# Optimization experiments

Measured on AMD Instinct MI355X. Metric: run time of the kernel, lower is better.

The kernel has to match this reference:

```python
import jax, jax.numpy as jnp
import numpy as np

BS, SL, FD = 8192, 49, 11
D_MODEL, DM2, HEAD = 128, 64, 8
NH, NHID, NLAYER = DM2 // HEAD, 4, 2
ABF = 1.0
XY_IDX = np.array([0, 1, 2, 3, 4, 5, 6, 7, 10])  # x feats + y feat (batch-normed cols)
DEC_IN = D_MODEL + 10  # d_model + len(x_dims + spa_dims)


def tanhshrink(x):
    return x - jnp.tanh(x)


def rope_angles(spa):
    # spa: [bs, sl, 2] -> per-token block angles [bs, sl, 4]
    # block order matches torch.block_diag(Rx(t0), Ry(t0), Rx(t1), Ry(t1))
    thetas = 10000.0 ** ((2.0 - 2.0 * jnp.arange(2, dtype=spa.dtype)) / 8.0)  # d=8, n_thetas=2
    ax = spa[..., 0:1] * thetas  # [bs, sl, 2]
    ay = spa[..., 1:2] * thetas
    return jnp.stack([ax[..., 0], ay[..., 0], ax[..., 1], ay[..., 1]], axis=-1)


def apply_rope(v, ang):
    # v: [bs, nh, s, 8]; ang: [bs, s, 4]. Applies the 8x8 block-diagonal
    # rotation directly on 2-d sub-pairs (same math as R @ v, no 8x8 matmats).
    c = jnp.cos(ang)[:, None]  # [bs, 1, s, 4]
    s = jnp.sin(ang)[:, None]
    v2 = v.reshape(*v.shape[:-1], 4, 2)
    r = jnp.stack([c * v2[..., 0] - s * v2[..., 1],
                   s * v2[..., 0] + c * v2[..., 1]], axis=-1)
    return r.reshape(v.shape)


def heads(x):  # [bs, s, dm2] -> [bs, nh, s, hd]
    b, s, _ = x.shape
    return x.reshape(b, s, NH, HEAD).transpose(0, 2, 1, 3)


def merge(x):  # [bs, nh, s, hd] -> [bs, s, dm2]
    b, h, s, d = x.shape
    return x.transpose(0, 2, 1, 3).reshape(b, s, h * d)


def mlp2(x, w1, b1, w2, b2):
    return tanhshrink(x @ w1 + b1) @ w2 + b2


def forward_impl(input_tensor, dists, bn_gamma, bn_beta,
                 xe_w1, xe_b1, xe_w2, xe_b2, ye_w1, ye_b1, ye_w2, ye_b2,
                 learnable_y, hidden_tokens, Wq, Wk, Wv, Wo, Wq2, Wk2, Wv2, Wo2,
                 dec_w0, dec_b0, dec_w1, dec_b1, dec_w2, dec_b2):
    bs = input_tensor.shape[0]
    # --- NanBatchNorm over x+y feature columns (no NaNs in clean inputs) ---
    xy = input_tensor[:, :, XY_IDX]
    mu = jnp.mean(xy, axis=(0, 1), keepdims=True)
    var = jnp.var(xy, axis=(0, 1), keepdims=True)
    xy = (xy - mu) / jnp.sqrt(var + 1e-5) * bn_gamma + bn_beta
    input_tensor = input_tensor.at[:, :, XY_IDX].set(xy)

    # --- target at last seq position: drop its dist, keep context dists ---
    dists_ctx = dists[:, :-1]                       # [bs, sl-1]
    central_x = input_tensor[:, -1:, :-1]           # [bs, 1, 10] (x + spa feats)

    # --- 2D RoPE angles from spatial coords ---
    ang = rope_angles(input_tensor[:, :, 8:10])     # [bs, sl, 4]

    # --- FCN encoders (two streams a=x, b=y) ---
    x_embed = mlp2(input_tensor[:, :, :8], xe_w1, xe_b1, xe_w2, xe_b2)      # [bs, sl, 64]
    y_embed = mlp2(input_tensor[:, :-1, 10:11], ye_w1, ye_b1, ye_w2, ye_b2)  # [bs, sl-1, 64]
    y_embed = jnp.concatenate([y_embed, jnp.broadcast_to(learnable_y, (bs, 1, DM2))], axis=1)

    ctx = (x_embed[:, :-1], y_embed[:, :-1])
    qry = (x_embed[:, -1:], y_embed[:, -1:])
    ang_ctx, ang_q = ang[:, :-1], ang[:, -1:]
    bias = (-ABF * dists_ctx)[:, None, None, :]     # [bs, 1, 1, sl-1]
    scale = 1.0 / jnp.sqrt(jnp.asarray(HEAD, input_tensor.dtype))

    outs, attn_ws = [], []
    for s in range(2):
        H = jnp.broadcast_to(hidden_tokens, (bs, NHID, DM2))
        for l in range(NLAYER):
            q = heads(H @ Wq[l, s])
            k = apply_rope(heads(ctx[s] @ Wk[l, s]), ang_ctx)
            v = heads(ctx[s] @ Wv[l, s])
            sc = jnp.einsum('bhqd,bhkd->bhqk', q, k) * scale + bias
            a = jax.nn.softmax(sc, axis=-1)
            H = H + merge(jnp.einsum('bhqk,bhkd->bhqd', a, v)) @ Wo[l, s]
        # query cross-attends the inducing tokens
        q = apply_rope(heads(qry[s] @ Wq2[s]), ang_q)
        k = heads(H @ Wk2[s])
        v = heads(H @ Wv2[s])
        sc = jnp.einsum('bhqd,bhkd->bhqk', q, k) * scale
        a = jax.nn.softmax(sc, axis=-1)
        outs.append(merge(jnp.einsum('bhqk,bhkd->bhqd', a, v)) @ Wo2[s])  # [bs, 1, 64]
        attn_ws.append(a)

    encoding = jnp.concatenate(outs, axis=-1)               # [bs, 1, 128]
    encoding = jnp.concatenate([encoding, central_x], axis=-1)  # [bs, 1, 138]
    h = tanhshrink(encoding @ dec_w0 + dec_b0)
    h = tanhshrink(h @ dec_w1 + dec_b1)
    pred = h @ dec_w2 + dec_b2                              # [bs, 1, 1]
    return pred


def setup_inputs() -> dict:
    key = jax.random.key(0)
    ks = jax.random.split(key, 32)
    g = lambda i, shape: 0.05 * jax.random.normal(ks[i], shape, dtype=jnp.float32)
    inp = {
        'input_tensor': jax.random.normal(ks[0], (BS, SL, FD), dtype=jnp.float32),
        'dists': jax.random.uniform(ks[1], (BS, SL), dtype=jnp.float32),
        'target_position': jnp.zeros((3, BS), dtype=jnp.int32),
        'bn_gamma': jnp.ones((9,), jnp.float32),
        'bn_beta': jnp.zeros((9,), jnp.float32),
        'xe_w1': g(2, (8, DM2)), 'xe_b1': jnp.zeros((DM2,), jnp.float32),
        'xe_w2': g(3, (DM2, DM2)), 'xe_b2': jnp.zeros((DM2,), jnp.float32),
        'ye_w1': g(4, (1, DM2)), 'ye_b1': jnp.zeros((DM2,), jnp.float32),
        'ye_w2': g(5, (DM2, DM2)), 'ye_b2': jnp.zeros((DM2,), jnp.float32),
        'learnable_y': g(6, (1, 1, DM2)),
        'hidden_tokens': g(7, (NHID, DM2)),
        'Wq': g(8, (NLAYER, 2, DM2, DM2)), 'Wk': g(9, (NLAYER, 2, DM2, DM2)),
        'Wv': g(10, (NLAYER, 2, DM2, DM2)), 'Wo': g(11, (NLAYER, 2, DM2, DM2)),
        'Wq2': g(12, (2, DM2, DM2)), 'Wk2': g(13, (2, DM2, DM2)),
        'Wv2': g(14, (2, DM2, DM2)), 'Wo2': g(15, (2, DM2, DM2)),
        'dec_w0': g(16, (DEC_IN, 512)), 'dec_b0': jnp.zeros((512,), jnp.float32),
        'dec_w1': g(17, (512, 256)), 'dec_b1': jnp.zeros((256,), jnp.float32),
        'dec_w2': g(18, (256, 1)), 'dec_b2': jnp.zeros((1,), jnp.float32),
    }
    return inp


def reference(input_tensor, dists, target_position, bn_gamma, bn_beta,
              xe_w1, xe_b1, xe_w2, xe_b2, ye_w1, ye_b1, ye_w2, ye_b2,
              learnable_y, hidden_tokens, Wq, Wk, Wv, Wo, Wq2, Wk2, Wv2, Wo2,
              dec_w0, dec_b0, dec_w1, dec_b1, dec_w2, dec_b2):
    # target_position is an index constant (query is the last token by construction)
    return forward_impl(input_tensor, dists, bn_gamma, bn_beta,
                        xe_w1, xe_b1, xe_w2, xe_b2, ye_w1, ye_b1, ye_w2, ye_b2,
                        learnable_y, hidden_tokens, Wq, Wk, Wv, Wo, Wq2, Wk2, Wv2, Wo2,
                        dec_w0, dec_b0, dec_w1, dec_b1, dec_w2, dec_b2)
```

## Files before the change

kernel.cpp:

```cpp
#include <hip/hip_runtime.h>
#include <math.h>

#define BS 8192
#define SL 49
#define FDIM 11
#define ROWS (BS*SL)

__device__ __forceinline__ float tanhshrink_f(float x) {
  float e = __expf(2.f * x);
  return (x - 1.f) + __fdividef(2.f, e + 1.f);
}

__global__ __launch_bounds__(256) void k_stats(const float* __restrict__ inp,
                                               double* __restrict__ gsum) {
  const int nblk = gridDim.x;
  const int per = (ROWS + nblk - 1) / nblk;
  const int r0 = blockIdx.x * per;
  int r1 = r0 + per; if (r1 > ROWS) r1 = ROWS;
  float s[9], q[9];
#pragma unroll
  for (int j = 0; j < 9; ++j) { s[j] = 0.f; q[j] = 0.f; }
  for (int r = r0 + threadIdx.x; r < r1; r += 256) {
    const float* row = inp + r * FDIM;
#pragma unroll
    for (int j = 0; j < 9; ++j) {
      float v = row[j < 8 ? j : 10];
      s[j] += v; q[j] += v * v;
    }
  }
#pragma unroll
  for (int j = 0; j < 9; ++j) {
    for (int off = 32; off; off >>= 1) {
      s[j] += __shfl_down(s[j], off);
      q[j] += __shfl_down(q[j], off);
    }
  }
  __shared__ float red[4][18];
  const int wid = threadIdx.x >> 6;
  const int lane = threadIdx.x & 63;
  if (lane == 0) {
#pragma unroll
    for (int j = 0; j < 9; ++j) { red[wid][j] = s[j]; red[wid][9 + j] = q[j]; }
  }
  __syncthreads();
  if (threadIdx.x < 18) {
    float t = red[0][threadIdx.x] + red[1][threadIdx.x] +
              red[2][threadIdx.x] + red[3][threadIdx.x];
    atomicAdd(&gsum[threadIdx.x], (double)t);
  }
}

__global__ __launch_bounds__(256) void k_finalize(const double* __restrict__ gsum,
                           const float* __restrict__ gamma,
                           const float* __restrict__ beta,
                           const float* __restrict__ hidden,
                           const float* __restrict__ Wq,
                           float* __restrict__ bnp,
                           float* __restrict__ q0g) {
  int tid = threadIdx.x;
  if (tid < 9) {
    const double N = (double)ROWS;
    double mean = gsum[tid] / N;
    double msq  = gsum[9 + tid] / N;
    float var = (float)(msq - mean * mean);
    float sc = gamma[tid] / sqrtf(var + 1e-5f);
    bnp[tid] = sc;
    bnp[9 + tid] = beta[tid] - (float)mean * sc;
  }
  int s = tid >> 7, i2 = (tid >> 6) & 1, c = tid & 63;
  const float* W = Wq + (s << 12);
#pragma unroll
  for (int ii = 0; ii < 2; ++ii) {
    int i = i2 + 2 * ii;
    float a = 0.f;
    for (int k = 0; k < 64; ++k) a += hidden[i * 64 + k] * W[k * 64 + c];
    q0g[s * 256 + i * 64 + c] = a;
  }
}

__global__ __launch_bounds__(256, 4) void k_mega(
    const float* __restrict__ inp, const float* __restrict__ dists,
    const float* __restrict__ bnp, const float* __restrict__ q0g,
    const float* __restrict__ xe_w1, const float* __restrict__ xe_b1,
    const float* __restrict__ xe_w2, const float* __restrict__ xe_b2,
    const float* __restrict__ ye_w1, const float* __restrict__ ye_b1,
    const float* __restrict__ ye_w2, const float* __restrict__ ye_b2,
    const float* __restrict__ learnable_y, const float* __restrict__ hidden_tokens,
    const float* __restrict__ Wq, const float* __restrict__ Wk,
    const float* __restrict__ Wv, const float* __restrict__ Wo,
    const float* __restrict__ Wq2, const float* __restrict__ Wk2,
    const float* __restrict__ Wv2, const float* __restrict__ Wo2,
    float* __restrict__ enc)
{
  __shared__ float raw[49][12];
  __shared__ float cs8[49][8];
  __shared__ float emb[49][64];
  __shared__ float KB[49][68];
  __shared__ float scb[32][52];
  __shared__ float Hs[4][64];
  __shared__ float qb[4][64];
  __shared__ float db[48];
  __shared__ float bnl[18];
  __shared__ float q2[64];
  __shared__ float o1[64];
  __shared__ float a2[32];

  const int tid  = threadIdx.x;
  const int lane = tid & 63;
  const int grp  = tid >> 6;
  const int b    = blockIdx.x >> 1;
  const int s    = blockIdx.x & 1;
  const float scale = 0.35355339059327373f;

  for (int i = tid; i < 49 * FDIM; i += 256) raw[i / FDIM][i % FDIM] = inp[b * (49*FDIM) + i];
  if (tid < 18) bnl[tid] = bnp[tid];
  if (tid >= 64 && tid < 112) db[tid - 64] = dists[b * 49 + (tid - 64)];
  __syncthreads();

  if (tid < 49) {
    float x = raw[tid][8], y = raw[tid][9];
    cs8[tid][0] = cosf(10.f * x); cs8[tid][1] = cosf(10.f * y);
    cs8[tid][2] = cosf(x);        cs8[tid][3] = cosf(y);
    cs8[tid][4] = sinf(10.f * x); cs8[tid][5] = sinf(10.f * y);
    cs8[tid][6] = sinf(x);        cs8[tid][7] = sinf(y);
  }
  for (int i = tid; i < 441; i += 256) {
    int t = i / 9, j = i - t * 9;
    int f = (j < 8) ? j : 10;
    raw[t][f] = raw[t][f] * bnl[j] + bnl[9 + j];
  }
  __syncthreads();

  if (s == 0 && tid < 10) enc[b * 138 + 128 + tid] = raw[48][tid];

  if (s == 0) {
    const float bias1 = xe_b1[lane];
    float acc[13];
#pragma unroll
    for (int j = 0; j < 13; ++j) acc[j] = bias1;
#pragma unroll
    for (int k = 0; k < 8; ++k) {
      float w = xe_w1[k * 64 + lane];
#pragma unroll
      for (int j = 0; j < 13; ++j) {
        int t = grp + 4 * j;
        if (t < 49) acc[j] += raw[t][k] * w;
      }
    }
#pragma unroll
    for (int j = 0; j < 13; ++j) {
      int t = grp + 4 * j;
      if (t < 49) KB[t][lane] = tanhshrink_f(acc[j]);
    }
  } else {
    const float w1y = ye_w1[lane];
    const float b1y = ye_b1[lane];
#pragma unroll
    for (int j = 0; j < 12; ++j) {
      int t = grp + 4 * j;
      KB[t][lane] = tanhshrink_f(raw[t][10] * w1y + b1y);
    }
  }

  if (s == 0) {
    const float b2 = xe_b2[lane];
    float acc[13];
#pragma unroll
    for (int j = 0; j < 13; ++j) acc[j] = b2;
    for (int k = 0; k < 64; k += 4) {
      float w0 = xe_w2[(k + 0) * 64 + lane];
      float w1_ = xe_w2[(k + 1) * 64 + lane];
      float w2_ = xe_w2[(k + 2) * 64 + lane];
      float w3_ = xe_w2[(k + 3) * 64 + lane];
#pragma unroll
      for (int j = 0; j < 13; ++j) {
        int t = grp + 4 * j;
        if (t < 49) {
          float4 cv = *(const float4*)&KB[t][k];
          acc[j] += cv.x * w0 + cv.y * w1_ + cv.z * w2_ + cv.w * w3_;
        }
      }
    }
#pragma unroll
    for (int j = 0; j < 13; ++j) {
      int t = grp + 4 * j;
      if (t < 49) emb[t][lane] = acc[j];
    }
  } else {
    const float b2 = ye_b2[lane];
    float acc[12];
#pragma unroll
    for (int j = 0; j < 12; ++j) acc[j] = b2;
    for (int k = 0; k < 64; k += 4) {
      float w0 = ye_w2[(k + 0) * 64 + lane];
      float w1_ = ye_w2[(k + 1) * 64 + lane];
      float w2_ = ye_w2[(k + 2) * 64 + lane];
      float w3_ = ye_w2[(k + 3) * 64 + lane];
#pragma unroll
      for (int j = 0; j < 12; ++j) {
        float4 cv = *(const float4*)&KB[grp + 4 * j][k];
        acc[j] += cv.x * w0 + cv.y * w1_ + cv.z * w2_ + cv.w * w3_;
      }
    }
#pragma unroll
    for (int j = 0; j < 12; ++j) emb[grp + 4 * j][lane] = acc[j];
    if (tid < 64) emb[48][lane] = learnable_y[lane];
  }
  Hs[grp][lane] = hidden_tokens[grp * 64 + lane];

#pragma unroll 1
  for (int l = 0; l < 2; ++l) {
    const float* Wk_p = Wk + ((l * 2 + s) << 12);
    const float* Wv_p = Wv + ((l * 2 + s) << 12);
    const float* Wo_p = Wo + ((l * 2 + s) << 12);
    if (l == 0) {
      qb[grp][lane] = q0g[s * 256 + tid];
    } else {
      const float* Wq_p = Wq + ((l * 2 + s) << 12);
      float a = 0.f;
      for (int k = 0; k < 64; k += 4) {
        float4 hv = *(const float4*)&Hs[grp][k];
        a += hv.x * Wq_p[(k + 0) * 64 + lane] + hv.y * Wq_p[(k + 1) * 64 + lane]
           + hv.z * Wq_p[(k + 2) * 64 + lane] + hv.w * Wq_p[(k + 3) * 64 + lane];
      }
      qb[grp][lane] = a;
    }
    {
      float aK[12];
#pragma unroll
      for (int j = 0; j < 12; ++j) aK[j] = 0.f;
      for (int k = 0; k < 64; k += 4) {
        float wk0 = Wk_p[(k + 0) * 64 + lane], wk1 = Wk_p[(k + 1) * 64 + lane];
        float wk2 = Wk_p[(k + 2) * 64 + lane], wk3 = Wk_p[(k + 3) * 64 + lane];
#pragma unroll
        for (int j = 0; j < 12; ++j) {
          float4 cv = *(const float4*)&emb[grp + 4 * j][k];
          aK[j] += cv.x * wk0 + cv.y * wk1 + cv.z * wk2 + cv.w * wk3;
        }
      }
      const int p = (lane >> 1) & 3;
      const int odd = lane & 1;
#pragma unroll
      for (int j = 0; j < 12; ++j) {
        int t = grp + 4 * j;
        float other = __shfl_xor(aK[j], 1);
        float co = cs8[t][p], si = cs8[t][4 + p];
        KB[t][lane] = odd ? (si * other + co * aK[j]) : (co * aK[j] - si * other);
      }
    }
    __syncthreads();
    {
      const int t0 = tid & 7;
      const int i  = (tid >> 3) & 3;
      const int h  = tid >> 5;
      const int r  = tid >> 3;
      float4 qa = *(const float4*)&qb[i][h * 8];
      float4 qc = *(const float4*)&qb[i][h * 8 + 4];
      float v[6];
#pragma unroll
      for (int j = 0; j < 6; ++j) {
        int t = t0 + 8 * j;
        float4 ka = *(const float4*)&KB[t][h * 8];
        float4 kc = *(const float4*)&KB[t][h * 8 + 4];
        float a = qa.x * ka.x + qa.y * ka.y + qa.z * ka.z + qa.w * ka.w
                + qc.x * kc.x + qc.y * kc.y + qc.z * kc.z + qc.w * kc.w;
        v[j] = a * scale - db[t];
      }
      float m = fmaxf(fmaxf(fmaxf(v[0], v[1]), fmaxf(v[2], v[3])), fmaxf(v[4], v[5]));
      m = fmaxf(m, __shfl_xor(m, 1));
      m = fmaxf(m, __shfl_xor(m, 2));
      m = fmaxf(m, __shfl_xor(m, 4));
      float sum = 0.f;
#pragma unroll
      for (int j = 0; j < 6; ++j) { v[j] = __expf(v[j] - m); sum += v[j]; }
      sum += __shfl_xor(sum, 1);
      sum += __shfl_xor(sum, 2);
      sum += __shfl_xor(sum, 4);
      float inv = 1.f / sum;
#pragma unroll
      for (int j = 0; j < 6; ++j) scb[r][t0 + 8 * j] = v[j] * inv;
    }
    __syncthreads();
    {
      float acc[8];
#pragma unroll
      for (int m = 0; m < 8; ++m) acc[m] = 0.f;
      for (int tt = 0; tt < 48; tt += 4) {
        float e0 = emb[tt + 0][lane], e1 = emb[tt + 1][lane];
        float e2 = emb[tt + 2][lane], e3 = emb[tt + 3][lane];
#pragma unroll
        for (int m = 0; m < 8; ++m) {
          float4 sc4 = *(const float4*)&scb[grp + 4 * m][tt];
          acc[m] += sc4.x * e0 + sc4.y * e1 + sc4.z * e2 + sc4.w * e3;
        }
      }
#pragma unroll
      for (int m = 0; m < 8; ++m) KB[grp + 4 * m][lane] = acc[m];
    }
    {
      const int r = ((lane >> 3) << 2) + grp;
      float a = 0.f;
      for (int c = 0; c < 64; c += 4) {
        float4 tv = *(const float4*)&KB[r][c];
        a += tv.x * Wv_p[(c + 0) * 64 + lane] + tv.y * Wv_p[(c + 1) * 64 + lane]
           + tv.z * Wv_p[(c + 2) * 64 + lane] + tv.w * Wv_p[(c + 3) * 64 + lane];
      }
      qb[grp][lane] = a;
    }
    {
      float a = Hs[grp][lane];
      for (int k = 0; k < 64; k += 4) {
        float4 av = *(const float4*)&qb[grp][k];
        a += av.x * Wo_p[(k + 0) * 64 + lane] + av.y * Wo_p[(k + 1) * 64 + lane]
           + av.z * Wo_p[(k + 2) * 64 + lane] + av.w * Wo_p[(k + 3) * 64 + lane];
      }
      Hs[grp][lane] = a;
    }
  }

  const float* Wq2_p = Wq2 + (s << 12);
  const float* Wk2_p = Wk2 + (s << 12);
  const float* Wv2_p = Wv2 + (s << 12);
  const float* Wo2_p = Wo2 + (s << 12);
  if (tid < 64) {
    float a = 0.f;
    for (int k = 0; k < 64; k += 4) {
      float4 cv = *(const float4*)&emb[48][k];
      a += cv.x * Wq2_p[(k + 0) * 64 + lane] + cv.y * Wq2_p[(k + 1) * 64 + lane]
         + cv.z * Wq2_p[(k + 2) * 64 + lane] + cv.w * Wq2_p[(k + 3) * 64 + lane];
    }
    float other = __shfl_xor(a, 1);
    int p = (lane >> 1) & 3;
    float co = cs8[48][p], si = cs8[48][4 + p];
    q2[lane] = (lane & 1) ? (si * other + co * a) : (co * a - si * other);
  }
  {
    float aK = 0.f, aV = 0.f;
    for (int k = 0; k < 64; k += 4) {
      float4 hv = *(const float4*)&Hs[grp][k];
      aK += hv.x * Wk2_p[(k + 0) * 64 + lane] + hv.y * Wk2_p[(k + 1) * 64 + lane]
          + hv.z * Wk2_p[(k + 2) * 64 + lane] + hv.w * Wk2_p[(k + 3) * 64 + lane];
      aV += hv.x * Wv2_p[(k + 0) * 64 + lane] + hv.y * Wv2_p[(k + 1) * 64 + lane]
          + hv.z * Wv2_p[(k + 2) * 64 + lane] + hv.w * Wv2_p[(k + 3) * 64 + lane];
    }
    KB[grp][lane] = aK;
    KB[8 + grp][lane] = aV;
  }
  __syncthreads();
  if (tid < 32) {
    int h = tid >> 2, i = tid & 3;
    float a = 0.f;
#pragma unroll
    for (int d = 0; d < 8; ++d) a += q2[h * 8 + d] * KB[i][h * 8 + d];
    a *= scale;
    float m = fmaxf(a, __shfl_xor(a, 1));
    m = fmaxf(m, __shfl_xor(m, 2));
    float e = __expf(a - m);
    float sum = e + __shfl_xor(e, 1);
    sum += __shfl_xor(sum, 2);
    a2[tid] = e / sum;
  }
  if (tid < 64) {
    int h = lane >> 3;
    float a = 0.f;
#pragma unroll
    for (int i = 0; i < 4; ++i) a += a2[h * 4 + i] * KB[8 + i][lane];
    o1[lane] = a;
  }
  if (tid < 64) {
    float a = 0.f;
    for (int k = 0; k < 64; k += 4) {
      float4 ov = *(const float4*)&o1[k];
      a += ov.x * Wo2_p[(k + 0) * 64 + lane] + ov.y * Wo2_p[(k + 1) * 64 + lane]
         + ov.z * Wo2_p[(k + 2) * 64 + lane] + ov.w * Wo2_p[(k + 3) * 64 + lane];
    }
    enc[b * 138 + s * 64 + lane] = a;
  }
}

__global__ __launch_bounds__(256, 5) void k_dec(
    const float* __restrict__ enc,
    const float* __restrict__ w0, const float* __restrict__ b0,
    const float* __restrict__ w1, const float* __restrict__ b1,
    const float* __restrict__ w2, const float* __restrict__ b2,
    float* __restrict__ out)
{
  __shared__ float encs[8][140];
  __shared__ float h0s[8][512];
  __shared__ float h1s[8][256];
  const int tid = threadIdx.x;
  const int rb = blockIdx.x * 8;

  for (int i = tid; i < 8 * 138; i += 256) {
    int r = i / 138, k = i - r * 138;
    encs[r][k] = enc[(rb + r) * 138 + k];
  }
  __syncthreads();
  {
    float acc0[8], acc1[8];
    const float bb0 = b0[tid], bb1 = b0[tid + 256];
#pragma unroll
    for (int r = 0; r < 8; ++r) { acc0[r] = bb0; acc1[r] = bb1; }
    for (int k = 0; k < 136; k += 4) {
      float wa0 = w0[(k + 0) * 512 + tid], wa1 = w0[(k + 1) * 512 + tid];
      float wa2 = w0[(k + 2) * 512 + tid], wa3 = w0[(k + 3) * 512 + tid];
      float wb0 = w0[(k + 0) * 512 + tid + 256], wb1 = w0[(k + 1) * 512 + tid + 256];
      float wb2 = w0[(k + 2) * 512 + tid + 256], wb3 = w0[(k + 3) * 512 + tid + 256];
#pragma unroll
      for (int r = 0; r < 8; ++r) {
        float4 ev = *(const float4*)&encs[r][k];
        acc0[r] += ev.x * wa0 + ev.y * wa1 + ev.z * wa2 + ev.w * wa3;
        acc1[r] += ev.x * wb0 + ev.y * wb1 + ev.z * wb2 + ev.w * wb3;
      }
    }
    for (int k = 136; k < 138; ++k) {
      float wa = w0[k * 512 + tid], wb = w0[k * 512 + tid + 256];
#pragma unroll
      for (int r = 0; r < 8; ++r) {
        float e = encs[r][k];
        acc0[r] += e * wa; acc1[r] += e * wb;
      }
    }
#pragma unroll
    for (int r = 0; r < 8; ++r) {
      h0s[r][tid] = tanhshrink_f(acc0[r]);
      h0s[r][tid + 256] = tanhshrink_f(acc1[r]);
    }
  }
  __syncthreads();
  {
    float acc[8];
    const float bb = b1[tid];
#pragma unroll
    for (int r = 0; r < 8; ++r) acc[r] = bb;
    for (int k = 0; k < 512; k += 4) {
      float ww0 = w1[(k + 0) * 256 + tid], ww1 = w1[(k + 1) * 256 + tid];
      float ww2 = w1[(k + 2) * 256 + tid], ww3 = w1[(k + 3) * 256 + tid];
#pragma unroll
      for (int r = 0; r < 8; ++r) {
        float4 hv = *(const float4*)&h0s[r][k];
        acc[r] += hv.x * ww0 + hv.y * ww1 + hv.z * ww2 + hv.w * ww3;
      }
    }
#pragma unroll
    for (int r = 0; r < 8; ++r) h1s[r][tid] = tanhshrink_f(acc[r]);
  }
  __syncthreads();
  {
    int r = tid >> 5, l32 = tid & 31;
    float a = 0.f;
#pragma unroll
    for (int kk = 0; kk < 8; ++kk) {
      int k = l32 + 32 * kk;
      a += h1s[r][k] * w2[k];
    }
    for (int off = 16; off; off >>= 1) a += __shfl_down(a, off, 32);
    if (l32 == 0) out[rb + r] = a + b2[0];
  }
}

extern "C" void kernel_launch(void* const* d_in, const int* in_sizes, int n_in,
                              void* d_out, int out_size, void* d_ws, size_t ws_size,
                              hipStream_t stream) {
  const float* inp        = (const float*)d_in[0];
  const float* dists      = (const float*)d_in[1];
  const float* bn_gamma   = (const float*)d_in[3];
  const float* bn_beta    = (const float*)d_in[4];
  const float* xe_w1      = (const float*)d_in[5];
  const float* xe_b1      = (const float*)d_in[6];
  const float* xe_w2      = (const float*)d_in[7];
  const float* xe_b2      = (const float*)d_in[8];
  const float* ye_w1      = (const float*)d_in[9];
  const float* ye_b1      = (const float*)d_in[10];
  const float* ye_w2      = (const float*)d_in[11];
  const float* ye_b2      = (const float*)d_in[12];
  const float* learnable  = (const float*)d_in[13];
  const float* hidden     = (const float*)d_in[14];
  const float* Wq         = (const float*)d_in[15];
  const float* Wk         = (const float*)d_in[16];
  const float* Wv         = (const float*)d_in[17];
  const float* Wo         = (const float*)d_in[18];
  const float* Wq2        = (const float*)d_in[19];
  const float* Wk2        = (const float*)d_in[20];
  const float* Wv2        = (const float*)d_in[21];
  const float* Wo2        = (const float*)d_in[22];
  const float* dec_w0     = (const float*)d_in[23];
  const float* dec_b0     = (const float*)d_in[24];
  const float* dec_w1     = (const float*)d_in[25];
  const float* dec_b1     = (const float*)d_in[26];
  const float* dec_w2     = (const float*)d_in[27];
  const float* dec_b2     = (const float*)d_in[28];

  double* gsum = (double*)d_ws;
  float*  bnp  = (float*)((char*)d_ws + 256);
  float*  q0g  = (float*)((char*)d_ws + 512);
  float*  enc  = (float*)((char*)d_ws + 2560);

  hipMemsetAsync(d_ws, 0, 256, stream);
  k_stats   <<<512, 256, 0, stream>>>(inp, gsum);
  k_finalize<<<1, 256, 0, stream>>>(gsum, bn_gamma, bn_beta, hidden, Wq, bnp, q0g);
  k_mega    <<<BS * 2, 256, 0, stream>>>(inp, dists, bnp, q0g,
                                         xe_w1, xe_b1, xe_w2, xe_b2,
                                         ye_w1, ye_b1, ye_w2, ye_b2,
                                         learnable, hidden,
                                         Wq, Wk, Wv, Wo, Wq2, Wk2, Wv2, Wo2, enc);
  k_dec     <<<BS / 8, 256, 0, stream>>>(enc, dec_w0, dec_b0, dec_w1, dec_b1,
                                         dec_w2, dec_b2, (float*)d_out);
}
```

Baseline: 987.6 us.

## Pre-transpose embedding and key weights; remap per-token matmuls to wave-uniform columns

k_finalize now writes transposed copies of the x/y encoder weights and Wk into workspace. In k_mega the embedding MLPs and key projection are remapped so each lane owns one token and each wave owns 16 output columns. With that mapping the weight reads are wave-uniform, contiguous float4 loads that can go through scalar/broadcast paths, and token rows are read from padded shared memory. The RoPE on keys becomes in-register pair rotation using a transposed cos/sin table, and extra block barriers are added. The cost is 16 float4 registers per lane, fewer active lanes (48-49 of 64), and a serial single-block transpose inside k_finalize.

```diff
diff --git a/kernel.cpp b/kernel.cpp
--- a/kernel.cpp
+++ b/kernel.cpp
@@ -55,8 +55,16 @@
                            const float* __restrict__ beta,
                            const float* __restrict__ hidden,
                            const float* __restrict__ Wq,
+                           const float* __restrict__ xe_w1,
+                           const float* __restrict__ xe_w2,
+                           const float* __restrict__ ye_w2,
+                           const float* __restrict__ Wk,
                            float* __restrict__ bnp,
-                           float* __restrict__ q0g) {
+                           float* __restrict__ q0g,
+                           float* __restrict__ xw1T,
+                           float* __restrict__ xw2T,
+                           float* __restrict__ yw2T,
+                           float* __restrict__ wkT) {
   int tid = threadIdx.x;
   if (tid < 9) {
     const double N = (double)ROWS;
@@ -76,25 +84,32 @@
     for (int k = 0; k < 64; ++k) a += hidden[i * 64 + k] * W[k * 64 + c];
     q0g[s * 256 + i * 64 + c] = a;
   }
+  for (int i = tid; i < 512; i += 256)  { int cc = i >> 3,  k = i & 7;  xw1T[i] = xe_w1[k * 64 + cc]; }
+  for (int i = tid; i < 4096; i += 256) { int cc = i >> 6,  k = i & 63; xw2T[i] = xe_w2[k * 64 + cc]; }
+  for (int i = tid; i < 4096; i += 256) { int cc = i >> 6,  k = i & 63; yw2T[i] = ye_w2[k * 64 + cc]; }
+  for (int i = tid; i < 16384; i += 256) {
+    int ls = i >> 12, r = i & 4095, cc = r >> 6, k = r & 63;
+    wkT[i] = Wk[ls * 4096 + k * 64 + cc];
+  }
 }
 
 __global__ __launch_bounds__(256, 4) void k_mega(
     const float* __restrict__ inp, const float* __restrict__ dists,
     const float* __restrict__ bnp, const float* __restrict__ q0g,
-    const float* __restrict__ xe_w1, const float* __restrict__ xe_b1,
-    const float* __restrict__ xe_w2, const float* __restrict__ xe_b2,
+    const float* __restrict__ xw1T, const float* __restrict__ xe_b1,
+    const float* __restrict__ xw2T, const float* __restrict__ xe_b2,
     const float* __restrict__ ye_w1, const float* __restrict__ ye_b1,
-    const float* __restrict__ ye_w2, const float* __restrict__ ye_b2,
+    const float* __restrict__ yw2T, const float* __restrict__ ye_b2,
     const float* __restrict__ learnable_y, const float* __restrict__ hidden_tokens,
-    const float* __restrict__ Wq, const float* __restrict__ Wk,
+    const float* __restrict__ Wq, const float* __restrict__ wkT,
     const float* __restrict__ Wv, const float* __restrict__ Wo,
     const float* __restrict__ Wq2, const float* __restrict__ Wk2,
     const float* __restrict__ Wv2, const float* __restrict__ Wo2,
     float* __restrict__ enc)
 {
   __shared__ float raw[49][12];
-  __shared__ float cs8[49][8];
-  __shared__ float emb[49][64];
+  __shared__ float cs8T[8][52];
+  __shared__ float embs[49 * 68];
   __shared__ float KB[49][68];
   __shared__ float scb[32][52];
   __shared__ float Hs[4][64];
@@ -108,6 +123,7 @@
   const int tid  = threadIdx.x;
   const int lane = tid & 63;
   const int grp  = tid >> 6;
+  const int wg   = __builtin_amdgcn_readfirstlane(grp);
   const int b    = blockIdx.x >> 1;
   const int s    = blockIdx.x & 1;
   const float scale = 0.35355339059327373f;
@@ -119,10 +135,10 @@
 
   if (tid < 49) {
     float x = raw[tid][8], y = raw[tid][9];
-    cs8[tid][0] = cosf(10.f * x); cs8[tid][1] = cosf(10.f * y);
-    cs8[tid][2] = cosf(x);        cs8[tid][3] = cosf(y);
-    cs8[tid][4] = sinf(10.f * x); cs8[tid][5] = sinf(10.f * y);
-    cs8[tid][6] = sinf(x);        cs8[tid][7] = sinf(y);
+    cs8T[0][tid] = cosf(10.f * x); cs8T[1][tid] = cosf(10.f * y);
+    cs8T[2][tid] = cosf(x);        cs8T[3][tid] = cosf(y);
+    cs8T[4][tid] = sinf(10.f * x); cs8T[5][tid] = sinf(10.f * y);
+    cs8T[6][tid] = sinf(x);        cs8T[7][tid] = sinf(y);
   }
   for (int i = tid; i < 441; i += 256) {
     int t = i / 9, j = i - t * 9;
@@ -134,83 +150,71 @@
   if (s == 0 && tid < 10) enc[b * 138 + 128 + tid] = raw[48][tid];
 
   if (s == 0) {
-    const float bias1 = xe_b1[lane];
-    float acc[13];
-#pragma unroll
-    for (int j = 0; j < 13; ++j) acc[j] = bias1;
-#pragma unroll
-    for (int k = 0; k < 8; ++k) {
-      float w = xe_w1[k * 64 + lane];
-#pragma unroll
-      for (int j = 0; j < 13; ++j) {
-        int t = grp + 4 * j;
-        if (t < 49) acc[j] += raw[t][k] * w;
-      }
-    }
-#pragma unroll
-    for (int j = 0; j < 13; ++j) {
-      int t = grp + 4 * j;
-      if (t < 49) KB[t][lane] = tanhshrink_f(acc[j]);
+    if (lane < 49) {
+      float4 r0 = *(const float4*)&raw[lane][0];
+      float4 r1 = *(const float4*)&raw[lane][4];
+      float h[16];
+#pragma unroll
+      for (int ci = 0; ci < 16; ++ci) {
+        int c = wg * 16 + ci;
+        const float* w = xw1T + c * 8;
+        float a = xe_b1[c]
+                + r0.x * w[0] + r0.y * w[1] + r0.z * w[2] + r0.w * w[3]
+                + r1.x * w[4] + r1.y * w[5] + r1.z * w[6] + r1.w * w[7];
+        h[ci] = tanhshrink_f(a);
+      }
+#pragma unroll
+      for (int i = 0; i < 4; ++i)
+        *(float4*)&KB[lane][wg * 16 + 4 * i] = make_float4(h[4*i], h[4*i+1], h[4*i+2], h[4*i+3]);
     }
   } else {
-    const float w1y = ye_w1[lane];
-    const float b1y = ye_b1[lane];
-#pragma unroll
-    for (int j = 0; j < 12; ++j) {
-      int t = grp + 4 * j;
-      KB[t][lane] = tanhshrink_f(raw[t][10] * w1y + b1y);
-    }
-  }
-
-  if (s == 0) {
-    const float b2 = xe_b2[lane];
-    float acc[13];
-#pragma unroll
-    for (int j = 0; j < 13; ++j) acc[j] = b2;
-    for (int k = 0; k < 64; k += 4) {
-      float w0 = xe_w2[(k + 0) * 64 + lane];
-      float w1_ = xe_w2[(k + 1) * 64 + lane];
-      float w2_ = xe_w2[(k + 2) * 64 + lane];
-      float w3_ = xe_w2[(k + 3) * 64 + lane];
-#pragma unroll
-      for (int j = 0; j < 13; ++j) {
-        int t = grp + 4 * j;
-        if (t < 49) {
-          float4 cv = *(const float4*)&KB[t][k];
-          acc[j] += cv.x * w0 + cv.y * w1_ + cv.z * w2_ + cv.w * w3_;
+    if (lane < 48) {
+      float ry = raw[lane][10];
+      float h[16];
+#pragma unroll
+      for (int ci = 0; ci < 16; ++ci) {
+        int c = wg * 16 + ci;
+        h[ci] = tanhshrink_f(ry * ye_w1[c] + ye_b1[c]);
+      }
+#pragma unroll
+      for (int i = 0; i < 4; ++i)
+        *(float4*)&KB[lane][wg * 16 + 4 * i] = make_float4(h[4*i], h[4*i+1], h[4*i+2], h[4*i+3]);
+    }
+  }
+  __syncthreads();
+
+  {
+    const int nrow = (s == 0) ? 49 : 48;
+    const float* WT = (s == 0) ? xw2T : yw2T;
+    const float* bb = (s == 0) ? xe_b2 : ye_b2;
+    if (lane < nrow) {
+      float4 h[16];
+#pragma unroll
+      for (int g = 0; g < 16; ++g) h[g] = *(const float4*)&KB[lane][4 * g];
+      float o[16];
+#pragma unroll
+      for (int ci = 0; ci < 16; ++ci) {
+        int c = wg * 16 + ci;
+        const float* w = WT + c * 64;
+        float a = bb[c];
+#pragma unroll
+        for (int g = 0; g < 16; ++g) {
+          float4 wv = *(const float4*)&w[4 * g];
+          a += h[g].x * wv.x + h[g].y * wv.y + h[g].z * wv.z + h[g].w * wv.w;
         }
-      }
-    }
-#pragma unroll
-    for (int j = 0; j < 13; ++j) {
-      int t = grp + 4 * j;
-      if (t < 49) emb[t][lane] = acc[j];
-    }
-  } else {
-    const float b2 = ye_b2[lane];
-    float acc[12];
-#pragma unroll
-    for (int j = 0; j < 12; ++j) acc[j] = b2;
-    for (int k = 0; k < 64; k += 4) {
-      float w0 = ye_w2[(k + 0) * 64 + lane];
-      float w1_ = ye_w2[(k + 1) * 64 + lane];
-      float w2_ = ye_w2[(k + 2) * 64 + lane];
-      float w3_ = ye_w2[(k + 3) * 64 + lane];
-#pragma unroll
-      for (int j = 0; j < 12; ++j) {
-        float4 cv = *(const float4*)&KB[grp + 4 * j][k];
-        acc[j] += cv.x * w0 + cv.y * w1_ + cv.z * w2_ + cv.w * w3_;
-      }
-    }
-#pragma unroll
-    for (int j = 0; j < 12; ++j) emb[grp + 4 * j][lane] = acc[j];
-    if (tid < 64) emb[48][lane] = learnable_y[lane];
+        o[ci] = a;
+      }
+#pragma unroll
+      for (int i = 0; i < 4; ++i)
+        *(float4*)&embs[lane * 68 + wg * 16 + 4 * i] = make_float4(o[4*i], o[4*i+1], o[4*i+2], o[4*i+3]);
+    }
+    if (s == 1 && tid < 64) embs[48 * 68 + lane] = learnable_y[lane];
   }
   Hs[grp][lane] = hidden_tokens[grp * 64 + lane];
+  __syncthreads();
 
 #pragma unroll 1
   for (int l = 0; l < 2; ++l) {
-    const float* Wk_p = Wk + ((l * 2 + s) << 12);
     const float* Wv_p = Wv + ((l * 2 + s) << 12);
     const float* Wo_p = Wo + ((l * 2 + s) << 12);
     if (l == 0) {
@@ -225,28 +229,35 @@
       }
       qb[grp][lane] = a;
     }
-    {
-      float aK[12];
-#pragma unroll
-      for (int j = 0; j < 12; ++j) aK[j] = 0.f;
-      for (int k = 0; k < 64; k += 4) {
-        float wk0 = Wk_p[(k + 0) * 64 + lane], wk1 = Wk_p[(k + 1) * 64 + lane];
-        float wk2 = Wk_p[(k + 2) * 64 + lane], wk3 = Wk_p[(k + 3) * 64 + lane];
-#pragma unroll
-        for (int j = 0; j < 12; ++j) {
-          float4 cv = *(const float4*)&emb[grp + 4 * j][k];
-          aK[j] += cv.x * wk0 + cv.y * wk1 + cv.z * wk2 + cv.w * wk3;
+    if (lane < 48) {
+      float4 e[16];
+#pragma unroll
+      for (int g = 0; g < 16; ++g) e[g] = *(const float4*)&embs[lane * 68 + 4 * g];
+      float kc[16];
+      const float* WTl = wkT + ((l * 2 + s) << 12);
+#pragma unroll
+      for (int ci = 0; ci < 16; ++ci) {
+        int c = wg * 16 + ci;
+        const float* w = WTl + c * 64;
+        float a = 0.f;
+#pragma unroll
+        for (int g = 0; g < 16; ++g) {
+          float4 wv = *(const float4*)&w[4 * g];
+          a += e[g].x * wv.x + e[g].y * wv.y + e[g].z * wv.z + e[g].w * wv.w;
         }
-      }
-      const int p = (lane >> 1) & 3;
-      const int odd = lane & 1;
-#pragma unroll
-      for (int j = 0; j < 12; ++j) {
-        int t = grp + 4 * j;
-        float other = __shfl_xor(aK[j], 1);
-        float co = cs8[t][p], si = cs8[t][4 + p];
-        KB[t][lane] = odd ? (si * other + co * aK[j]) : (co * aK[j] - si * other);
-      }
+        kc[ci] = a;
+      }
+      float ko[16];
+#pragma unroll
+      for (int i = 0; i < 8; ++i) {
+        int p = (8 * wg + i) & 3;
+        float co = cs8T[p][lane], si = cs8T[4 + p][lane];
+        ko[2*i]   = co * kc[2*i] - si * kc[2*i+1];
+        ko[2*i+1] = si * kc[2*i] + co * kc[2*i+1];
+      }
+#pragma unroll
+      for (int i = 0; i < 4; ++i)
+        *(float4*)&KB[lane][wg * 16 + 4 * i] = make_float4(ko[4*i], ko[4*i+1], ko[4*i+2], ko[4*i+3]);
     }
     __syncthreads();
     {
@@ -286,8 +297,8 @@
 #pragma unroll
       for (int m = 0; m < 8; ++m) acc[m] = 0.f;
       for (int tt = 0; tt < 48; tt += 4) {
-        float e0 = emb[tt + 0][lane], e1 = emb[tt + 1][lane];
-        float e2 = emb[tt + 2][lane], e3 = emb[tt + 3][lane];
+        float e0 = embs[(tt + 0) * 68 + lane], e1 = embs[(tt + 1) * 68 + lane];
+        float e2 = embs[(tt + 2) * 68 + lane], e3 = embs[(tt + 3) * 68 + lane];
 #pragma unroll
         for (int m = 0; m < 8; ++m) {
           float4 sc4 = *(const float4*)&scb[grp + 4 * m][tt];
@@ -316,6 +327,7 @@
       }
       Hs[grp][lane] = a;
     }
+    if (l == 0) __syncthreads();
   }
 
   const float* Wq2_p = Wq2 + (s << 12);
@@ -325,13 +337,13 @@
   if (tid < 64) {
     float a = 0.f;
     for (int k = 0; k < 64; k += 4) {
-      float4 cv = *(const float4*)&emb[48][k];
+      float4 cv = *(const float4*)&embs[48 * 68 + k];
       a += cv.x * Wq2_p[(k + 0) * 64 + lane] + cv.y * Wq2_p[(k + 1) * 64 + lane]
          + cv.z * Wq2_p[(k + 2) * 64 + lane] + cv.w * Wq2_p[(k + 3) * 64 + lane];
     }
     float other = __shfl_xor(a, 1);
     int p = (lane >> 1) & 3;
-    float co = cs8[48][p], si = cs8[48][4 + p];
+    float co = cs8T[p][48], si = cs8T[4 + p][48];
     q2[lane] = (lane & 1) ? (si * other + co * a) : (co * a - si * other);
   }
   {
@@ -495,15 +507,21 @@
   float*  bnp  = (float*)((char*)d_ws + 256);
   float*  q0g  = (float*)((char*)d_ws + 512);
   float*  enc  = (float*)((char*)d_ws + 2560);
+  float*  xw1T = (float*)((char*)d_ws + 4524544);
+  float*  xw2T = (float*)((char*)d_ws + 4526592);
+  float*  yw2T = (float*)((char*)d_ws + 4542976);
+  float*  wkT  = (float*)((char*)d_ws + 4559360);
 
   hipMemsetAsync(d_ws, 0, 256, stream);
   k_stats   <<<512, 256, 0, stream>>>(inp, gsum);
-  k_finalize<<<1, 256, 0, stream>>>(gsum, bn_gamma, bn_beta, hidden, Wq, bnp, q0g);
+  k_finalize<<<1, 256, 0, stream>>>(gsum, bn_gamma, bn_beta, hidden, Wq,
+                                    xe_w1, xe_w2, ye_w2, Wk,
+                                    bnp, q0g, xw1T, xw2T, yw2T, wkT);
   k_mega    <<<BS * 2, 256, 0, stream>>>(inp, dists, bnp, q0g,
-                                         xe_w1, xe_b1, xe_w2, xe_b2,
-                                         ye_w1, ye_b1, ye_w2, ye_b2,
+                                         xw1T, xe_b1, xw2T, xe_b2,
+                                         ye_w1, ye_b1, yw2T, ye_b2,
                                          learnable, hidden,
-                                         Wq, Wk, Wv, Wo, Wq2, Wk2, Wv2, Wo2, enc);
+                                         Wq, wkT, Wv, Wo, Wq2, Wk2, Wv2, Wo2, enc);
   k_dec     <<<BS / 8, 256, 0, stream>>>(enc, dec_w0, dec_b0, dec_w1, dec_b1,
                                          dec_w2, dec_b2, (float*)d_out);
 }
```

Measured after the change: 2.635 ms. 2.67x slower.
